# Kernel tuning notes

Measured on AMD Instinct MI355X. Metric: run time of the kernel, lower is better.

Reference implementation:

```python
import jax, jax.numpy as jnp
import numpy as np

D = 128
N = 50000
E = 600000


def setup_inputs() -> dict:
    key = jax.random.key(0)
    ks = jax.random.split(key, 6)
    x_a = jax.random.normal(ks[0], (N, D), dtype=jnp.float32)
    x_b = jax.random.normal(ks[1], (N, D), dtype=jnp.float32)
    ei_ab = jax.random.randint(ks[2], (2, E), 0, N)  # row0: src in 'a', row1: dst in 'b'
    ei_ba = jax.random.randint(ks[3], (2, E), 0, N)  # row0: src in 'b', row1: dst in 'a'
    scale = 1.0 / np.sqrt(D).astype(np.float32)
    # [layer, node_type(a,b), q/k/v, D, D]
    qkv_w = jax.random.normal(ks[4], (2, 2, 3, D, D), dtype=jnp.float32) * scale
    qkv_b = jnp.zeros((2, 2, 3, D), dtype=jnp.float32)
    # [layer, edge_type(ab,ba), D, D] -- bilinear attention weights
    edge_W = jax.random.normal(ks[5], (2, 2, D, D), dtype=jnp.float32) * scale
    return {"x_a": x_a, "x_b": x_b, "ei_ab": ei_ab, "ei_ba": ei_ba,
            "qkv_w": qkv_w, "qkv_b": qkv_b, "edge_W": edge_W}


def _edge_attend(q, k, v, W, src, dst, n_dst):
    """Bilinear per-edge attention + segment softmax over dst + scatter-add."""
    d = q.shape[-1]
    qW = q @ W                                   # [N_src, D] (node-level, cheap)
    s = jnp.sum(qW[src] * k[dst], axis=-1) / jnp.sqrt(jnp.asarray(d, q.dtype))  # [E]
    s = jax.nn.leaky_relu(s, negative_slope=0.01)
    m = jax.ops.segment_max(s, dst, num_segments=n_dst)      # per-dst max
    e = jnp.exp(s - m[dst])
    denom = jax.ops.segment_sum(e, dst, num_segments=n_dst)
    alpha = e / denom[dst]                                   # [E]
    return jax.ops.segment_sum(alpha[:, None] * v[src], dst, num_segments=n_dst)


def _layer(x_a, x_b, ei_ab, ei_ba, w, b, eW):
    # w: [2 types, 3, D, D]; b: [2, 3, D]; eW: [2 edge types, D, D]
    q_a, k_a, v_a = [x_a @ w[0, i] + b[0, i] for i in range(3)]
    q_b, k_b, v_b = [x_b @ w[1, i] + b[1, i] for i in range(3)]
    # edge type a->b: q/v from src type 'a', k from dst type 'b'
    out_b = _edge_attend(q_a, k_b, v_a, eW[0], ei_ab[0], ei_ab[1], x_b.shape[0])
    # edge type b->a: q/v from src type 'b', k from dst type 'a'
    out_a = _edge_attend(q_b, k_a, v_b, eW[1], ei_ba[0], ei_ba[1], x_a.shape[0])
    return out_a, out_b


def reference(x_a, x_b, ei_ab, ei_ba, qkv_w, qkv_b, edge_W):
    h_a, h_b = _layer(x_a, x_b, ei_ab, ei_ba, qkv_w[0], qkv_b[0], edge_W[0])
    h_a = jax.nn.relu(h_a)
    h_b = jax.nn.relu(h_b)
    o_a, o_b = _layer(h_a, h_b, ei_ab, ei_ba, qkv_w[1], qkv_b[1], edge_W[1])
    return o_a, o_b
```

## Files before the change

### kernel.cpp

```cpp
#include <hip/hip_runtime.h>
#include <math.h>

#define DD 128
#define CHUNK 8192
#define CAP 5120

typedef __attribute__((ext_vector_type(8))) short bf16x8;
typedef __attribute__((ext_vector_type(4))) float f32x4;

__device__ __forceinline__ ushort f2bf(float f) {
    union { float f; unsigned u; } v; v.f = f;
    unsigned r = v.u + 0x7fff + ((v.u >> 16) & 1);
    return (ushort)(r >> 16);
}

__device__ __forceinline__ float2 bfp(unsigned u) {
    union { unsigned x; float f; } a, b;
    a.x = u << 16;
    b.x = u & 0xffff0000u;
    return make_float2(a.f, b.f);
}

__global__ __launch_bounds__(256) void combine_all(const float* __restrict__ qkv_w,
                                                   const float* __restrict__ qkv_b,
                                                   const float* __restrict__ edge_W,
                                                   float* __restrict__ WC,
                                                   float* __restrict__ BCq)
{
    const int z = blockIdx.y;
    const int L = z >> 1, t = z & 1;
    const float* wq = qkv_w + (((size_t)L * 2 + t) * 3 + 0) * DD * DD;
    const float* bq = qkv_b + (((size_t)L * 2 + t) * 3 + 0) * DD;
    const float* We = edge_W + ((size_t)L * 2 + t) * DD * DD;
    float* Wz = WC + (size_t)z * DD * DD;
    float* Bz = BCq + (size_t)z * DD;

    const int tid = threadIdx.x;
    const int i = blockIdx.x * 2 + (tid >> 7);
    const int j = tid & 127;
    float sum = 0.f;
    for (int k = 0; k < DD; ++k) sum = fmaf(wq[i * DD + k], We[k * DD + j], sum);
    Wz[i * DD + j] = sum;
    if (blockIdx.x == 0 && tid < DD) {
        float s2 = 0.f;
        for (int k = 0; k < DD; ++k) s2 = fmaf(bq[k], We[k * DD + j], s2);
        Bz[j] = s2;
    }
}

__global__ __launch_bounds__(256) void pack_all(const float* __restrict__ qkv_w,
                                                const float* __restrict__ qkv_b,
                                                const float* __restrict__ WC,
                                                const float* __restrict__ BCq,
                                                ushort* __restrict__ W3P,
                                                float* __restrict__ B3)
{
    const int z = blockIdx.y;
    const int L = z >> 1, t = z & 1;
    const int ci = blockIdx.x * 256 + threadIdx.x;
    const int cb = ci >> 11;
    const int ct = (ci >> 8) & 7;
    const int ks = (ci >> 6) & 3;
    const int l  = ci & 63;
    const int c3 = cb * 128 + ct * 16 + (l & 15);
    const int k0 = ks * 32 + (l >> 4) * 8;

    const float* wv = qkv_w + (((size_t)L * 2 + t) * 3 + 2) * DD * DD;
    const float* wk = qkv_w + (((size_t)L * 2 + t) * 3 + 1) * DD * DD;
    const float* src;
    int cc;
    if (c3 < 128)      { src = WC + (size_t)z * DD * DD; cc = c3; }
    else if (c3 < 256) { src = wv; cc = c3 - 128; }
    else               { src = wk; cc = c3 - 256; }

    ushort h[8];
    #pragma unroll
    for (int j = 0; j < 8; ++j) h[j] = f2bf(src[(size_t)(k0 + j) * DD + cc]);
    ushort* dst = W3P + (size_t)z * 6144 * 8 + (size_t)ci * 8;
    #pragma unroll
    for (int j = 0; j < 8; ++j) dst[j] = h[j];

    if (ci < 384) {
        float bv;
        if (ci < 128)      bv = BCq[(size_t)z * DD + ci];
        else if (ci < 256) bv = qkv_b[(((size_t)L * 2 + t) * 3 + 2) * DD + (ci - 128)];
        else               bv = qkv_b[(((size_t)L * 2 + t) * 3 + 1) * DD + (ci - 256)];
        B3[(size_t)z * 384 + ci] = bv;
    }
}

template<bool F32_IN, bool RELU_IN>
__global__ __launch_bounds__(256, 4) void gemm_mfma(const void* __restrict__ Xav,
                                                    const void* __restrict__ Xbv,
                                                    const ushort* __restrict__ WpL,
                                                    const float* __restrict__ bL,
                                                    ushort* __restrict__ QVa,
                                                    ushort* __restrict__ FKa,
                                                    ushort* __restrict__ QVb,
                                                    ushort* __restrict__ FKb,
                                                    int N)
{
    const int t = (blockIdx.y >= 3) ? 1 : 0;
    const int p = blockIdx.y - t * 3;
    ushort* QV = t ? QVb : QVa;
    ushort* FK = t ? FKb : FKa;
    const ushort* Bp = WpL + (size_t)t * 49152 + (size_t)p * 16384;
    const float* bz = bL + t * 384 + p * 128;
    ushort* outp   = (p == 2) ? FK : QV;
    const int stride = (p == 2) ? 128 : 256;
    const int off    = (p == 1) ? 128 : 0;

    __shared__ ushort Bs[16384];

    const int tid  = threadIdx.x;
    const int wave = tid >> 6;
    const int lane = tid & 63;
    const int row0 = blockIdx.x * 64 + wave * 16;
    const int arow = row0 + (lane & 15);
    const bool aok = arow < N;
    const int kcol = (lane >> 4) * 8;

    #pragma unroll
    for (int i = 0; i < 8; ++i) {
        const int c = tid + i * 256;
        *(float4*)&Bs[(size_t)c * 8] = ((const float4*)Bp)[c];
    }

    bf16x8 a[4];
    if (F32_IN) {
        const float* X = (const float*)(t ? Xbv : Xav);
        const float* xr = X + (size_t)arow * DD + kcol;
        #pragma unroll
        for (int ks = 0; ks < 4; ++ks) {
            bf16x8 h = (bf16x8){0,0,0,0,0,0,0,0};
            if (aok) {
                float4 v0 = *(const float4*)&xr[ks * 32];
                float4 v1 = *(const float4*)&xr[ks * 32 + 4];
                h[0]=(short)f2bf(v0.x); h[1]=(short)f2bf(v0.y); h[2]=(short)f2bf(v0.z); h[3]=(short)f2bf(v0.w);
                h[4]=(short)f2bf(v1.x); h[5]=(short)f2bf(v1.y); h[6]=(short)f2bf(v1.z); h[7]=(short)f2bf(v1.w);
            }
            a[ks] = h;
        }
    } else {
        const ushort* X = (const ushort*)(t ? Xbv : Xav);
        const ushort* xr = X + (size_t)arow * DD + kcol;
        #pragma unroll
        for (int ks = 0; ks < 4; ++ks) {
            bf16x8 h = (bf16x8){0,0,0,0,0,0,0,0};
            if (aok) h = *(const bf16x8*)&xr[ks * 32];
            if (RELU_IN) {
                #pragma unroll
                for (int j = 0; j < 8; ++j)
                    h[j] = (short)(((ushort)h[j] & 0x8000u) ? 0 : (ushort)h[j]);
            }
            a[ks] = h;
        }
    }
    __syncthreads();

    f32x4 acc[8];
    #pragma unroll
    for (int ct = 0; ct < 8; ++ct) {
        acc[ct] = (f32x4){0.f, 0.f, 0.f, 0.f};
        #pragma unroll
        for (int ks = 0; ks < 4; ++ks) {
            bf16x8 b = *(const bf16x8*)&Bs[(size_t)((ct * 4 + ks) * 64 + lane) * 8];
            acc[ct] = __builtin_amdgcn_mfma_f32_16x16x32_bf16(a[ks], b, acc[ct], 0, 0, 0);
        }
    }

    const int rbase = row0 + (lane >> 4) * 4;
    #pragma unroll
    for (int ct = 0; ct < 8; ++ct) {
        const int col = ct * 16 + (lane & 15);
        const float bv = bz[col];
        #pragma unroll
        for (int j = 0; j < 4; ++j) {
            const int rr = rbase + j;
            if (rr < N) outp[(size_t)rr * stride + off + col] = f2bf(acc[ct][j] + bv);
        }
    }
}

__global__ __launch_bounds__(256) void zero_ints(int* __restrict__ p, int n)
{
    int i = blockIdx.x * 256 + threadIdx.x;
    if (i < n) p[i] = 0;
}

__global__ __launch_bounds__(256) void bkt_hist(const int* __restrict__ dst0,
                                                const int* __restrict__ dst1,
                                                int* __restrict__ bcnt, int nE)
{
    const int t = blockIdx.y;
    const int* dst = t ? dst1 : dst0;
    __shared__ int h[256];
    h[threadIdx.x] = 0;
    __syncthreads();
    for (int e = blockIdx.x * 256 + threadIdx.x; e < nE; e += gridDim.x * 256)
        atomicAdd(&h[dst[e] >> 8], 1);
    __syncthreads();
    if (h[threadIdx.x]) atomicAdd(&bcnt[t * 256 + threadIdx.x], h[threadIdx.x]);
}

__global__ __launch_bounds__(64) void bkt_scan(const int* __restrict__ bcnt,
                                               int* __restrict__ bbase,
                                               int* __restrict__ bcur,
                                               int* __restrict__ offs0,
                                               int* __restrict__ offs1, int N, int nE)
{
    if (threadIdx.x < 2) {
        int t = threadIdx.x;
        int run = 0;
        for (int i = 0; i < 256; ++i) {
            int v = bcnt[t * 256 + i];
            bbase[t * 256 + i] = run;
            bcur[t * 256 + i] = run;
            run += v;
        }
        if (t == 0) offs0[N] = nE; else offs1[N] = nE;
    }
}

__global__ __launch_bounds__(256) void bkt_part(const int* __restrict__ src0,
                                                const int* __restrict__ dst0,
                                                const int* __restrict__ src1,
                                                const int* __restrict__ dst1,
                                                int* __restrict__ bcur,
                                                unsigned* __restrict__ stage0,
                                                unsigned* __restrict__ stage1,
                                                int nE, int nbkt)
{
    const int t = blockIdx.y;
    const int* src = t ? src1 : src0;
    const int* dst = t ? dst1 : dst0;
    unsigned* stage = t ? stage1 : stage0;
    int* bc = bcur + t * 256;

    __shared__ unsigned ebuf[CHUNK];
    __shared__ int cnt[256], loff[256], cur[256], resv[256];

    const int tid  = threadIdx.x;
    const int e0   = blockIdx.x * CHUNK;
    const int ecnt = min(CHUNK, nE - e0);

    cnt[tid] = 0;
    __syncthreads();

    unsigned pk[CHUNK / 256];
    #pragma unroll
    for (int i = 0; i < CHUNK / 256; ++i) {
        const int le = i * 256 + tid;
        unsigned p = 0xFFFFFFFFu;
        if (le < ecnt) {
            int d = dst[e0 + le], s = src[e0 + le];
            p = ((unsigned)(d >> 8) << 24) | ((unsigned)(d & 255) << 16) | (unsigned)s;
            atomicAdd(&cnt[d >> 8], 1);
        }
        pk[i] = p;
    }
    __syncthreads();

    int v = cnt[tid];
    loff[tid] = v;
    __syncthreads();
    for (int off = 1; off < 256; off <<= 1) {
        int a = (tid >= off) ? loff[tid - off] : 0;
        __syncthreads();
        loff[tid] += a;
        __syncthreads();
    }
    int excl = loff[tid] - v;
    __syncthreads();
    loff[tid] = excl;
    cur[tid]  = excl;
    __syncthreads();

    #pragma unroll
    for (int i = 0; i < CHUNK / 256; ++i) {
        unsigned p = pk[i];
        if (p != 0xFFFFFFFFu) {
            int b = p >> 24;
            int pos = atomicAdd(&cur[b], 1);
            ebuf[pos] = p;
        }
    }
    __syncthreads();

    if (tid < nbkt && cnt[tid] > 0) resv[tid] = atomicAdd(&bc[tid], cnt[tid]);
    __syncthreads();

    const int wv = tid >> 6, ln = tid & 63;
    for (int b = wv; b < nbkt; b += 4) {
        const int c = cnt[b];
        if (c == 0) continue;
        const int lo = loff[b];
        const int rb = resv[b];
        for (int i = ln; i < c; i += 64) stage[rb + i] = ebuf[lo + i];
    }
}

__global__ __launch_bounds__(256) void bkt_fill(const unsigned* __restrict__ stage0,
                                                const unsigned* __restrict__ stage1,
                                                const int* __restrict__ bcnt,
                                                const int* __restrict__ bbase,
                                                int* __restrict__ offs0,
                                                int* __restrict__ offs1,
                                                int* __restrict__ col0,
                                                int* __restrict__ col1, int N)
{
    const int b = blockIdx.x, t = blockIdx.y;
    const unsigned* stage = t ? stage1 : stage0;
    int* offs = t ? offs1 : offs0;
    int* col  = t ? col1 : col0;
    const int base = bbase[t * 256 + b];
    int cb = bcnt[t * 256 + b];
    if (cb > CAP) cb = CAP;

    __shared__ unsigned ebuf[CAP];
    __shared__ int colbuf[CAP];
    __shared__ int dcnt[256], doff[256], dcur[256];

    const int tid = threadIdx.x;
    dcnt[tid] = 0;
    __syncthreads();

    for (int i = tid; i < cb; i += 256) {
        unsigned p = stage[base + i];
        ebuf[i] = p;
        atomicAdd(&dcnt[(p >> 16) & 255], 1);
    }
    __syncthreads();

    int v = dcnt[tid];
    doff[tid] = v;
    __syncthreads();
    for (int off = 1; off < 256; off <<= 1) {
        int a = (tid >= off) ? doff[tid - off] : 0;
        __syncthreads();
        doff[tid] += a;
        __syncthreads();
    }
    int excl = doff[tid] - v;
    dcur[tid] = excl;
    const int node = (b << 8) + tid;
    if (node < N) offs[node] = base + excl;
    __syncthreads();

    for (int i = tid; i < cb; i += 256) {
        unsigned p = ebuf[i];
        int pos = atomicAdd(&dcur[(p >> 16) & 255], 1);
        colbuf[pos] = (int)(p & 0xFFFFu);
    }
    __syncthreads();

    for (int i = tid; i < cb; i += 256) col[base + i] = colbuf[i];
}

template<bool BF16_OUT>
__global__ __launch_bounds__(256) void attn_gather(const ushort* __restrict__ QV,
                                                   const ushort* __restrict__ K,
                                                   const int* __restrict__ offs,
                                                   const int* __restrict__ col,
                                                   void* __restrict__ outv, int n)
{
    const int wid  = (blockIdx.x * 256 + threadIdx.x) >> 6;
    const int lane = threadIdx.x & 63;
    if (wid >= n) return;
    const int li = lane & 15;
    const int g  = lane >> 4;

    const int beg = offs[wid], end = offs[wid + 1];

    uint4 ku = ((const uint4*)(K + (size_t)wid * DD))[li];
    float kf[8];
    {
        float2 t;
        t = bfp(ku.x); kf[0]=t.x; kf[1]=t.y;
        t = bfp(ku.y); kf[2]=t.x; kf[3]=t.y;
        t = bfp(ku.z); kf[4]=t.x; kf[5]=t.y;
        t = bfp(ku.w); kf[6]=t.x; kf[7]=t.y;
    }

    float m = -__builtin_inff();
    float den = 0.f;
    float acc[8] = {0.f,0.f,0.f,0.f,0.f,0.f,0.f,0.f};

    int p = beg + g;
    uint4 qn = make_uint4(0,0,0,0), vn = make_uint4(0,0,0,0);
    if (p < end) {
        const ushort* row = QV + (size_t)col[p] * 256;
        qn = ((const uint4*)row)[li];
        vn = ((const uint4*)(row + 128))[li];
    }

    while (p < end) {
        uint4 qu = qn, vu = vn;
        const int pn = p + 4;
        if (pn < end) {
            const ushort* row = QV + (size_t)col[pn] * 256;
            qn = ((const uint4*)row)[li];
            vn = ((const uint4*)(row + 128))[li];
        }
        float2 t;
        float d;
        t = bfp(qu.x); d  = t.x*kf[0] + t.y*kf[1];
        t = bfp(qu.y); d += t.x*kf[2] + t.y*kf[3];
        t = bfp(qu.z); d += t.x*kf[4] + t.y*kf[5];
        t = bfp(qu.w); d += t.x*kf[6] + t.y*kf[7];
        d += __shfl_xor(d, 1);
        d += __shfl_xor(d, 2);
        d += __shfl_xor(d, 4);
        d += __shfl_xor(d, 8);
        float sc = d * 0.08838834764831845f;
        sc = sc > 0.f ? sc : 0.01f * sc;
        float nm = fmaxf(m, sc);
        float f  = __expf(m - nm);
        float pe = __expf(sc - nm);
        den = den * f + pe;
        float2 v0 = bfp(vu.x), v1 = bfp(vu.y), v2 = bfp(vu.z), v3 = bfp(vu.w);
        acc[0] = acc[0]*f + pe*v0.x;  acc[1] = acc[1]*f + pe*v0.y;
        acc[2] = acc[2]*f + pe*v1.x;  acc[3] = acc[3]*f + pe*v1.y;
        acc[4] = acc[4]*f + pe*v2.x;  acc[5] = acc[5]*f + pe*v2.y;
        acc[6] = acc[6]*f + pe*v3.x;  acc[7] = acc[7]*f + pe*v3.y;
        m = nm;
        p = pn;
    }

    float m1 = fmaxf(m, __shfl_xor(m, 16));
    float m2 = fmaxf(m1, __shfl_xor(m1, 32));
    float f = (den > 0.f) ? __expf(m - m2) : 0.f;
    den *= f;
    den += __shfl_xor(den, 16);
    den += __shfl_xor(den, 32);
    #pragma unroll
    for (int j = 0; j < 8; ++j) {
        acc[j] *= f;
        acc[j] += __shfl_xor(acc[j], 16);
        acc[j] += __shfl_xor(acc[j], 32);
    }
    if (g == 0) {
        const float inv = den > 0.f ? 1.f / den : 0.f;
        if (BF16_OUT) {
            ushort* o = (ushort*)outv + (size_t)wid * DD + li * 8;
            bf16x8 h;
            #pragma unroll
            for (int j = 0; j < 8; ++j) h[j] = (short)f2bf(acc[j] * inv);
            *(bf16x8*)o = h;
        } else {
            float* o = (float*)outv + (size_t)wid * DD + li * 8;
            *(float4*)o       = make_float4(acc[0]*inv, acc[1]*inv, acc[2]*inv, acc[3]*inv);
            *(float4*)(o + 4) = make_float4(acc[4]*inv, acc[5]*inv, acc[6]*inv, acc[7]*inv);
        }
    }
}

extern "C" void kernel_launch(void* const* d_in, const int* in_sizes, int n_in,
                              void* d_out, int out_size, void* d_ws, size_t ws_size,
                              hipStream_t stream)
{
    const float* x_a    = (const float*)d_in[0];
    const float* x_b    = (const float*)d_in[1];
    const int*   ei_ab  = (const int*)d_in[2];
    const int*   ei_ba  = (const int*)d_in[3];
    const float* qkv_w  = (const float*)d_in[4];
    const float* qkv_b  = (const float*)d_in[5];
    const float* edge_W = (const float*)d_in[6];
    float* out = (float*)d_out;

    const int N = in_sizes[0] / DD;
    const int E = in_sizes[2] / 2;
    const int nbkt = (N + 255) >> 8;

    float* ws = (float*)d_ws;
    float* WC  = ws;
    float* BCq = WC + 4 * DD * DD;
    float* B3  = BCq + 4 * DD;
    ushort* W3P = (ushort*)(B3 + 4 * 384);
    ushort* HA  = W3P + (size_t)4 * 49152;
    ushort* HB  = HA + (size_t)N * DD;
    ushort* QVa = HB + (size_t)N * DD;
    ushort* QVb = QVa + (size_t)N * 256;
    ushort* FKa = QVb + (size_t)N * 256;
    ushort* FKb = FKa + (size_t)N * DD;
    int* ip      = (int*)(FKb + (size_t)N * DD);
    int* bcnt    = ip;
    int* bbase   = bcnt + 512;
    int* bcur    = bbase + 512;
    int* offs_ab = bcur + 512;
    int* offs_ba = offs_ab + (N + 1);
    int* col_ab  = offs_ba + (N + 1);
    int* col_ba  = col_ab + E;
    unsigned* stage0 = (unsigned*)(col_ba + E);
    unsigned* stage1 = stage0 + E;

    {
        dim3 g1(64, 4);
        combine_all<<<g1, 256, 0, stream>>>(qkv_w, qkv_b, edge_W, WC, BCq);
        dim3 g2(24, 4);
        pack_all<<<g2, 256, 0, stream>>>(qkv_w, qkv_b, WC, BCq, W3P, B3);
    }

    const int* s_ab = ei_ab;  const int* d_ab = ei_ab + E;
    const int* s_ba = ei_ba;  const int* d_ba = ei_ba + E;
    {
        zero_ints<<<2, 256, 0, stream>>>(bcnt, 512);
        dim3 hg(128, 2);
        bkt_hist<<<hg, 256, 0, stream>>>(d_ab, d_ba, bcnt, E);
        bkt_scan<<<1, 64, 0, stream>>>(bcnt, bbase, bcur, offs_ab, offs_ba, N, E);
        dim3 pg((E + CHUNK - 1) / CHUNK, 2);
        bkt_part<<<pg, 256, 0, stream>>>(s_ab, d_ab, s_ba, d_ba, bcur,
                                         stage0, stage1, E, nbkt);
        dim3 fg(nbkt, 2);
        bkt_fill<<<fg, 256, 0, stream>>>(stage0, stage1, bcnt, bbase,
                                         offs_ab, offs_ba, col_ab, col_ba, N);
    }

    const dim3 gemm_grid((N + 63) / 64, 6);
    const int ag_grid = (N + 3) / 4;

    gemm_mfma<true, false><<<gemm_grid, 256, 0, stream>>>(
        x_a, x_b, W3P, B3, QVa, FKa, QVb, FKb, N);
    attn_gather<true><<<ag_grid, 256, 0, stream>>>(QVa, FKb, offs_ab, col_ab, HB, N);
    attn_gather<true><<<ag_grid, 256, 0, stream>>>(QVb, FKa, offs_ba, col_ba, HA, N);

    float* o_a = out;
    float* o_b = out + (size_t)N * DD;
    gemm_mfma<false, true><<<gemm_grid, 256, 0, stream>>>(
        HA, HB, W3P + (size_t)2 * 49152, B3 + 2 * 384, QVa, FKa, QVb, FKb, N);
    attn_gather<false><<<ag_grid, 256, 0, stream>>>(QVa, FKb, offs_ab, col_ab, o_b, N);
    attn_gather<false><<<ag_grid, 256, 0, stream>>>(QVb, FKa, offs_ba, col_ba, o_a, N);
}
```

Measured before the change: 344.7 us.

## Process four row tiles per GEMM block with double-buffered A loads

Each GEMM block now covers 256 rows instead of 64, with each wave working through four 16-row tiles. This spreads the 32KB weight-slice load into shared memory over four times more output rows. A-fragment loads for the next tile are interleaved with the MFMA compute of the current one to hide global latency, and bias values are hoisted into registers. The cost is a quarter as many blocks (about 196 per projection), which lowers occupancy and parallelism, and higher register pressure from the two A buffers.

```diff
diff --git a/kernel.cpp b/kernel.cpp
--- a/kernel.cpp
+++ b/kernel.cpp
@@ -112,13 +112,12 @@
 
     __shared__ ushort Bs[16384];
 
-    const int tid  = threadIdx.x;
-    const int wave = tid >> 6;
-    const int lane = tid & 63;
-    const int row0 = blockIdx.x * 64 + wave * 16;
-    const int arow = row0 + (lane & 15);
-    const bool aok = arow < N;
-    const int kcol = (lane >> 4) * 8;
+    const int tid   = threadIdx.x;
+    const int wave  = tid >> 6;
+    const int lane  = tid & 63;
+    const int wrow0 = blockIdx.x * 256 + wave * 64;
+    const int rlane = lane & 15;
+    const int kcol  = (lane >> 4) * 8;
 
     #pragma unroll
     for (int i = 0; i < 8; ++i) {
@@ -126,60 +125,91 @@
         *(float4*)&Bs[(size_t)c * 8] = ((const float4*)Bp)[c];
     }
 
-    bf16x8 a[4];
-    if (F32_IN) {
-        const float* X = (const float*)(t ? Xbv : Xav);
-        const float* xr = X + (size_t)arow * DD + kcol;
-        #pragma unroll
-        for (int ks = 0; ks < 4; ++ks) {
-            bf16x8 h = (bf16x8){0,0,0,0,0,0,0,0};
-            if (aok) {
-                float4 v0 = *(const float4*)&xr[ks * 32];
-                float4 v1 = *(const float4*)&xr[ks * 32 + 4];
-                h[0]=(short)f2bf(v0.x); h[1]=(short)f2bf(v0.y); h[2]=(short)f2bf(v0.z); h[3]=(short)f2bf(v0.w);
-                h[4]=(short)f2bf(v1.x); h[5]=(short)f2bf(v1.y); h[6]=(short)f2bf(v1.z); h[7]=(short)f2bf(v1.w);
-            }
-            a[ks] = h;
-        }
-    } else {
-        const ushort* X = (const ushort*)(t ? Xbv : Xav);
-        const ushort* xr = X + (size_t)arow * DD + kcol;
-        #pragma unroll
-        for (int ks = 0; ks < 4; ++ks) {
-            bf16x8 h = (bf16x8){0,0,0,0,0,0,0,0};
-            if (aok) h = *(const bf16x8*)&xr[ks * 32];
-            if (RELU_IN) {
-                #pragma unroll
-                for (int j = 0; j < 8; ++j)
-                    h[j] = (short)(((ushort)h[j] & 0x8000u) ? 0 : (ushort)h[j]);
-            }
-            a[ks] = h;
-        }
-    }
-    __syncthreads();
-
-    f32x4 acc[8];
-    #pragma unroll
-    for (int ct = 0; ct < 8; ++ct) {
-        acc[ct] = (f32x4){0.f, 0.f, 0.f, 0.f};
-        #pragma unroll
-        for (int ks = 0; ks < 4; ++ks) {
-            bf16x8 b = *(const bf16x8*)&Bs[(size_t)((ct * 4 + ks) * 64 + lane) * 8];
-            acc[ct] = __builtin_amdgcn_mfma_f32_16x16x32_bf16(a[ks], b, acc[ct], 0, 0, 0);
-        }
-    }
-
-    const int rbase = row0 + (lane >> 4) * 4;
-    #pragma unroll
-    for (int ct = 0; ct < 8; ++ct) {
-        const int col = ct * 16 + (lane & 15);
-        const float bv = bz[col];
-        #pragma unroll
-        for (int j = 0; j < 4; ++j) {
-            const int rr = rbase + j;
-            if (rr < N) outp[(size_t)rr * stride + off + col] = f2bf(acc[ct][j] + bv);
-        }
-    }
+    const float* Xf = (const float*)(t ? Xbv : Xav);
+    const ushort* Xh = (const ushort*)(t ? Xbv : Xav);
+
+    float bvs[8];
+    #pragma unroll
+    for (int ct = 0; ct < 8; ++ct) bvs[ct] = bz[ct * 16 + rlane];
+
+#define LOAD_A(TILE, DST)                                                        \
+    {                                                                            \
+        const int arow = wrow0 + (TILE) * 16 + rlane;                            \
+        const bool aok = arow < N;                                               \
+        if (F32_IN) {                                                            \
+            const float* xr = Xf + (size_t)arow * DD + kcol;                     \
+            _Pragma("unroll")                                                    \
+            for (int ks = 0; ks < 4; ++ks) {                                     \
+                bf16x8 h = (bf16x8){0,0,0,0,0,0,0,0};                            \
+                if (aok) {                                                       \
+                    float4 v0 = *(const float4*)&xr[ks * 32];                    \
+                    float4 v1 = *(const float4*)&xr[ks * 32 + 4];                \
+                    h[0]=(short)f2bf(v0.x); h[1]=(short)f2bf(v0.y);              \
+                    h[2]=(short)f2bf(v0.z); h[3]=(short)f2bf(v0.w);              \
+                    h[4]=(short)f2bf(v1.x); h[5]=(short)f2bf(v1.y);              \
+                    h[6]=(short)f2bf(v1.z); h[7]=(short)f2bf(v1.w);              \
+                }                                                                \
+                DST[ks] = h;                                                     \
+            }                                                                    \
+        } else {                                                                 \
+            const ushort* xr = Xh + (size_t)arow * DD + kcol;                    \
+            _Pragma("unroll")                                                    \
+            for (int ks = 0; ks < 4; ++ks) {                                     \
+                bf16x8 h = (bf16x8){0,0,0,0,0,0,0,0};                            \
+                if (aok) h = *(const bf16x8*)&xr[ks * 32];                       \
+                if (RELU_IN) {                                                   \
+                    _Pragma("unroll")                                            \
+                    for (int j = 0; j < 8; ++j)                                  \
+                        h[j] = (short)(((ushort)h[j] & 0x8000u) ? 0              \
+                                        : (ushort)h[j]);                         \
+                }                                                                \
+                DST[ks] = h;                                                     \
+            }                                                                    \
+        }                                                                        \
+    }
+
+#define COMPUTE_STORE(TILE, A)                                                   \
+    {                                                                            \
+        f32x4 acc[8];                                                            \
+        _Pragma("unroll")                                                        \
+        for (int ct = 0; ct < 8; ++ct) {                                         \
+            acc[ct] = (f32x4){0.f, 0.f, 0.f, 0.f};                               \
+            _Pragma("unroll")                                                    \
+            for (int ks = 0; ks < 4; ++ks) {                                     \
+                bf16x8 b = *(const bf16x8*)&Bs[(size_t)((ct * 4 + ks) * 64       \
+                                                        + lane) * 8];            \
+                acc[ct] = __builtin_amdgcn_mfma_f32_16x16x32_bf16(A[ks], b,      \
+                                                                  acc[ct],0,0,0);\
+            }                                                                    \
+        }                                                                        \
+        const int rbase = wrow0 + (TILE) * 16 + (lane >> 4) * 4;                 \
+        _Pragma("unroll")                                                        \
+        for (int ct = 0; ct < 8; ++ct) {                                         \
+            const int col = ct * 16 + rlane;                                     \
+            _Pragma("unroll")                                                    \
+            for (int j = 0; j < 4; ++j) {                                        \
+                const int rr = rbase + j;                                        \
+                if (rr < N)                                                      \
+                    outp[(size_t)rr * stride + off + col]                        \
+                        = f2bf(acc[ct][j] + bvs[ct]);                            \
+            }                                                                    \
+        }                                                                        \
+    }
+
+    bf16x8 a0[4], a1[4];
+    LOAD_A(0, a0);
+    __syncthreads();
+
+    LOAD_A(1, a1);
+    COMPUTE_STORE(0, a0);
+    LOAD_A(2, a0);
+    COMPUTE_STORE(1, a1);
+    LOAD_A(3, a1);
+    COMPUTE_STORE(2, a0);
+    COMPUTE_STORE(3, a1);
+
+#undef LOAD_A
+#undef COMPUTE_STORE
 }
 
 __global__ __launch_bounds__(256) void zero_ints(int* __restrict__ p, int n)
@@ -516,7 +546,7 @@
                                          offs_ab, offs_ba, col_ab, col_ba, N);
     }
 
-    const dim3 gemm_grid((N + 63) / 64, 6);
+    const dim3 gemm_grid((N + 255) / 256, 6);
     const int ag_grid = (N + 3) / 4;
 
     gemm_mfma<true, false><<<gemm_grid, 256, 0, stream>>>(
```

Measured after the change: 426.2 us. +23.6%, slower.

## Reuse loaded input rows across all three projections and vectorize output stores

Applied to the files above, without the earlier changes.

The projection GEMM now launches one block per node tile and type and loops over the three weight matrices inside the block. Each input row is therefore loaded and converted to bf16 once instead of three times. The MFMA operands are swapped so each lane holds four consecutive output columns, which allows packed 4-element bf16 stores and float4 bias loads. In exchange the grid has one third as many blocks, and each block serializes three weight-tile loads into shared memory with extra barriers.

```diff
diff --git a/kernel.cpp b/kernel.cpp
--- a/kernel.cpp
+++ b/kernel.cpp
@@ -7,6 +7,7 @@
 
 typedef __attribute__((ext_vector_type(8))) short bf16x8;
 typedef __attribute__((ext_vector_type(4))) float f32x4;
+typedef __attribute__((ext_vector_type(4))) unsigned short u16x4;
 
 __device__ __forceinline__ ushort f2bf(float f) {
     union { float f; unsigned u; } v; v.f = f;
@@ -100,84 +101,90 @@
                                                     ushort* __restrict__ FKb,
                                                     int N)
 {
-    const int t = (blockIdx.y >= 3) ? 1 : 0;
-    const int p = blockIdx.y - t * 3;
+    const int t = blockIdx.y;
     ushort* QV = t ? QVb : QVa;
     ushort* FK = t ? FKb : FKa;
-    const ushort* Bp = WpL + (size_t)t * 49152 + (size_t)p * 16384;
-    const float* bz = bL + t * 384 + p * 128;
-    ushort* outp   = (p == 2) ? FK : QV;
-    const int stride = (p == 2) ? 128 : 256;
-    const int off    = (p == 1) ? 128 : 0;
-
-    __shared__ ushort Bs[16384];
+    const ushort* Wz = WpL + (size_t)t * 49152;
+    const float* bz0 = bL + t * 384;
+
+    __shared__ ushort Ws[16384];
 
     const int tid  = threadIdx.x;
     const int wave = tid >> 6;
     const int lane = tid & 63;
-    const int row0 = blockIdx.x * 64 + wave * 16;
-    const int arow = row0 + (lane & 15);
-    const bool aok = arow < N;
-    const int kcol = (lane >> 4) * 8;
-
-    #pragma unroll
-    for (int i = 0; i < 8; ++i) {
-        const int c = tid + i * 256;
-        *(float4*)&Bs[(size_t)c * 8] = ((const float4*)Bp)[c];
-    }
-
-    bf16x8 a[4];
+    const int node = blockIdx.x * 64 + wave * 16 + (lane & 15);
+    const bool ok  = node < N;
+    const int kc   = (lane >> 4) * 8;
+    const int frow = (lane >> 4) * 4;
+
+    bf16x8 x[4];
     if (F32_IN) {
         const float* X = (const float*)(t ? Xbv : Xav);
-        const float* xr = X + (size_t)arow * DD + kcol;
+        const float* xr = X + (size_t)node * DD + kc;
         #pragma unroll
         for (int ks = 0; ks < 4; ++ks) {
             bf16x8 h = (bf16x8){0,0,0,0,0,0,0,0};
-            if (aok) {
+            if (ok) {
                 float4 v0 = *(const float4*)&xr[ks * 32];
                 float4 v1 = *(const float4*)&xr[ks * 32 + 4];
                 h[0]=(short)f2bf(v0.x); h[1]=(short)f2bf(v0.y); h[2]=(short)f2bf(v0.z); h[3]=(short)f2bf(v0.w);
                 h[4]=(short)f2bf(v1.x); h[5]=(short)f2bf(v1.y); h[6]=(short)f2bf(v1.z); h[7]=(short)f2bf(v1.w);
             }
-            a[ks] = h;
+            x[ks] = h;
         }
     } else {
         const ushort* X = (const ushort*)(t ? Xbv : Xav);
-        const ushort* xr = X + (size_t)arow * DD + kcol;
+        const ushort* xr = X + (size_t)node * DD + kc;
         #pragma unroll
         for (int ks = 0; ks < 4; ++ks) {
             bf16x8 h = (bf16x8){0,0,0,0,0,0,0,0};
-            if (aok) h = *(const bf16x8*)&xr[ks * 32];
+            if (ok) h = *(const bf16x8*)&xr[ks * 32];
             if (RELU_IN) {
                 #pragma unroll
                 for (int j = 0; j < 8; ++j)
                     h[j] = (short)(((ushort)h[j] & 0x8000u) ? 0 : (ushort)h[j]);
             }
-            a[ks] = h;
-        }
-    }
-    __syncthreads();
-
-    f32x4 acc[8];
+            x[ks] = h;
+        }
+    }
+
     #pragma unroll
-    for (int ct = 0; ct < 8; ++ct) {
-        acc[ct] = (f32x4){0.f, 0.f, 0.f, 0.f};
+    for (int p = 0; p < 3; ++p) {
+        if (p) __syncthreads();
         #pragma unroll
-        for (int ks = 0; ks < 4; ++ks) {
-            bf16x8 b = *(const bf16x8*)&Bs[(size_t)((ct * 4 + ks) * 64 + lane) * 8];
-            acc[ct] = __builtin_amdgcn_mfma_f32_16x16x32_bf16(a[ks], b, acc[ct], 0, 0, 0);
-        }
-    }
-
-    const int rbase = row0 + (lane >> 4) * 4;
-    #pragma unroll
-    for (int ct = 0; ct < 8; ++ct) {
-        const int col = ct * 16 + (lane & 15);
-        const float bv = bz[col];
+        for (int i = 0; i < 8; ++i) {
+            const int c = tid + i * 256;
+            *(float4*)&Ws[(size_t)c * 8] = ((const float4*)(Wz + (size_t)p * 16384))[c];
+        }
+        __syncthreads();
+
+        f32x4 acc[8];
         #pragma unroll
-        for (int j = 0; j < 4; ++j) {
-            const int rr = rbase + j;
-            if (rr < N) outp[(size_t)rr * stride + off + col] = f2bf(acc[ct][j] + bv);
+        for (int ct = 0; ct < 8; ++ct) {
+            acc[ct] = (f32x4){0.f, 0.f, 0.f, 0.f};
+            #pragma unroll
+            for (int ks = 0; ks < 4; ++ks) {
+                bf16x8 w = *(const bf16x8*)&Ws[(size_t)((ct * 4 + ks) * 64 + lane) * 8];
+                acc[ct] = __builtin_amdgcn_mfma_f32_16x16x32_bf16(w, x[ks], acc[ct], 0, 0, 0);
+            }
+        }
+
+        if (ok) {
+            ushort* outp   = (p == 2) ? FK : QV;
+            const int stride = (p == 2) ? 128 : 256;
+            const int off    = (p == 1) ? 128 : 0;
+            const float* bzp = bz0 + p * 128;
+            ushort* orow = outp + (size_t)node * stride + off;
+            #pragma unroll
+            for (int ct = 0; ct < 8; ++ct) {
+                const float4 bv = *(const float4*)&bzp[ct * 16 + frow];
+                u16x4 o;
+                o[0] = f2bf(acc[ct][0] + bv.x);
+                o[1] = f2bf(acc[ct][1] + bv.y);
+                o[2] = f2bf(acc[ct][2] + bv.z);
+                o[3] = f2bf(acc[ct][3] + bv.w);
+                *(u16x4*)&orow[ct * 16 + frow] = o;
+            }
         }
     }
 }
@@ -516,7 +523,7 @@
                                          offs_ab, offs_ba, col_ab, col_ba, N);
     }
 
-    const dim3 gemm_grid((N + 63) / 64, 6);
+    const dim3 gemm_grid((N + 63) / 64, 2);
     const int ag_grid = (N + 3) / 4;
 
     gemm_mfma<true, false><<<gemm_grid, 256, 0, stream>>>(
```

Result: faster. 321.2 us (-6.8%).
